# Optimization experiments

Measured on AMD Instinct MI355X. Metric: run time of the kernel, lower is better.

The kernel has to match this reference:

```python
import jax, jax.numpy as jnp
import numpy as np

N, E = 50000, 1000000
IN_DIM, HID, OUT = 2, 32, 16
H1, H2 = 4, 1
NEG_SLOPE = 0.2
LN_EPS = 1e-5


def _glorot(key, shape):
    fan_in, fan_out = shape[0], shape[1]
    lim = (6.0 / (fan_in + fan_out)) ** 0.5
    return jax.random.uniform(key, shape, jnp.float32, -lim, lim)


def layer_norm(x, g, b):
    mu = jnp.mean(x, axis=-1, keepdims=True)
    var = jnp.var(x, axis=-1, keepdims=True)
    return (x - mu) * jax.lax.rsqrt(var + LN_EPS) * g + b


def gatv2_conv(x, src, dst, edge_attr, Wl, bl, Wr, br, We, att, bias, H, C):
    # x: (N, F) -> out: (N, C)  (concat=False: mean over heads)
    n = x.shape[0]
    xl = (x @ Wl + bl).reshape(n, H, C)   # source transform
    xr = (x @ Wr + br).reshape(n, H, C)   # destination transform
    e = (edge_attr @ We).reshape(-1, H, C)  # edge feature transform (no bias)
    # per-edge message, LeakyReLU, attention logit
    m = jax.nn.leaky_relu(xl[src] + xr[dst] + e, NEG_SLOPE)  # (E, H, C)
    logit = jnp.einsum('ehc,hc->eh', m, att)                 # (E, H)
    # scatter softmax grouped by destination node
    amax = jax.ops.segment_max(logit, dst, num_segments=n)    # (N, H)
    ex = jnp.exp(logit - amax[dst])                           # (E, H)
    denom = jax.ops.segment_sum(ex, dst, num_segments=n)      # (N, H)
    alpha = ex / (denom[dst] + 1e-16)                         # (E, H)
    # weighted scatter-aggregate of source features
    out = jax.ops.segment_sum(alpha[:, :, None] * xl[src], dst, num_segments=n)  # (N, H, C)
    return jnp.mean(out, axis=1) + bias


def setup_inputs() -> dict:
    key = jax.random.key(0)
    ks = jax.random.split(key, 16)
    x = jax.random.normal(ks[0], (N, IN_DIM), jnp.float32)
    edge_index = jax.random.randint(ks[1], (2, E), 0, N, jnp.int64)
    edge_attr = jax.random.normal(ks[2], (E, 1), jnp.float32)
    inp = {
        'x': x, 'edge_index': edge_index, 'edge_attr': edge_attr,
        # layer 1 (in=2 -> H1*HID)
        'W1l': _glorot(ks[3], (IN_DIM, H1 * HID)), 'b1l': jnp.zeros((H1 * HID,), jnp.float32),
        'W1r': _glorot(ks[4], (IN_DIM, H1 * HID)), 'b1r': jnp.zeros((H1 * HID,), jnp.float32),
        'We1': _glorot(ks[5], (1, H1 * HID)),
        'att1': _glorot(ks[6], (H1, HID)),
        'bias1': jnp.zeros((HID,), jnp.float32),
        'g1': jnp.ones((HID,), jnp.float32), 'beta1': jnp.zeros((HID,), jnp.float32),
        # layer 2 (HID -> H2*OUT)
        'W2l': _glorot(ks[7], (HID, H2 * OUT)), 'b2l': jnp.zeros((H2 * OUT,), jnp.float32),
        'W2r': _glorot(ks[8], (HID, H2 * OUT)), 'b2r': jnp.zeros((H2 * OUT,), jnp.float32),
        'We2': _glorot(ks[9], (1, H2 * OUT)),
        'att2': _glorot(ks[10], (H2, OUT)),
        'bias2': jnp.zeros((OUT,), jnp.float32),
        'g2': jnp.ones((OUT,), jnp.float32), 'beta2': jnp.zeros((OUT,), jnp.float32),
    }
    return inp


def reference(x, edge_index, edge_attr, W1l, b1l, W1r, b1r, We1, att1, bias1, g1, beta1,
              W2l, b2l, W2r, b2r, We2, att2, bias2, g2, beta2):
    src, dst = edge_index[0], edge_index[1]
    h = gatv2_conv(x, src, dst, edge_attr, W1l, b1l, W1r, b1r, We1, att1, bias1, H1, HID)
    h = jax.nn.elu(layer_norm(h, g1, beta1))  # dropout p=0.0 -> identity
    z = gatv2_conv(h, src, dst, edge_attr, W2l, b2l, W2r, b2r, We2, att2, bias2, H2, OUT)
    return layer_norm(z, g2, beta2)
```

## Files before the change

kernel.cpp:

```cpp
#include <hip/hip_runtime.h>
#include <hip/hip_bf16.h>
#include <math.h>

typedef __hip_bfloat16 bf16;

__device__ __forceinline__ float b2f(bf16 v) { return __bfloat162float(v); }
__device__ __forceinline__ bf16  f2b(float v) { return __float2bfloat16(v); }

template<int F32>
__device__ __forceinline__ float ldf(const void* p, int i) {
    return F32 ? ((const float*)p)[i] : b2f(((const bf16*)p)[i]);
}
template<int F32>
__device__ __forceinline__ void ldx(const void* x, int s, float& x0, float& x1) {
    if (F32) { float2 v = ((const float2*)x)[s]; x0 = v.x; x1 = v.y; }
    else {
        unsigned u = ((const unsigned*)x)[s];
        x0 = __uint_as_float((u & 0xFFFFu) << 16);
        x1 = __uint_as_float(u & 0xFFFF0000u);
    }
}
__device__ __forceinline__ unsigned f2b_hi(float f) {
    unsigned u = __float_as_uint(f);
    u += 0x7FFFu + ((u >> 16) & 1u);
    return u & 0xFFFF0000u;
}
template<int P4>
__device__ __forceinline__ void ldrec(const void* csr, int k, int& s, float& a) {
    if (P4) {
        unsigned u = ((const unsigned*)csr)[k];
        s = (int)(u & 0xFFFFu);
        a = __uint_as_float(u & 0xFFFF0000u);
    } else {
        uint2 r = ((const uint2*)csr)[k];
        s = (int)r.x;
        a = __uint_as_float(r.y);
    }
}
__device__ __forceinline__ float sclamp(float v, float lim) {
    return fminf(fmaxf(v, -lim), lim);
}
template<int CTRL>
__device__ __forceinline__ float dpp_add(float v) {
    int t = __builtin_amdgcn_update_dpp(0, __float_as_int(v), CTRL, 0xF, 0xF, true);
    return v + __int_as_float(t);
}
__device__ __forceinline__ float red16(float v) {
    v = dpp_add<0xB1>(v);
    v = dpp_add<0x4E>(v);
    v = dpp_add<0x124>(v);
    v = dpp_add<0x128>(v);
    return v;
}

#define NEG_SLOPE 0.2f
#define LN_EPS 1e-5f
#define SCAN_TILE 1024
#define ACHUNK 4096

__device__ __forceinline__ int ld_idx(const int* ei, long long pos, int is64, int N) {
    int v = is64 ? ei[2 * pos] : ei[pos];
    return min(max(v, 0), N - 1);
}
__device__ __forceinline__ int calc_is64(const int* ei) {
    int hi = 0, nz = 0;
    #pragma unroll
    for (int i = 0; i < 8; ++i) { hi |= ei[2 * i + 1]; nz |= ei[2 * i]; }
    return (hi == 0 && nz != 0) ? 1 : 0;
}


__global__ __launch_bounds__(256) void histb_kernel(const int* __restrict__ ei,
                                                    const unsigned short* __restrict__ xu,
                                                    int E, int N, int* __restrict__ flags,
                                                    int* __restrict__ bcnt) {
    __shared__ int c[256];
    int tid = threadIdx.x;
    c[tid] = 0;
    int is64 = calc_is64(ei);
    if (blockIdx.x == 0 && tid == 0) {
        flags[0] = is64;
        int pl = 0;
        for (int i = 0; i < 32; ++i) {
            unsigned ex = (xu[2 * i] >> 7) & 0xFF;
            if (ex >= 100 && ex <= 140) pl++;
        }
        flags[1] = (pl >= 24) ? 0 : 1;
    }
    __syncthreads();
    int i0 = blockIdx.x * ACHUNK;
    int iend = min(i0 + ACHUNK, E);
    for (int i = i0 + tid; i < iend; i += 256)
        atomicAdd(&c[ld_idx(ei, (long long)E + i, is64, N) >> 8], 1);
    __syncthreads();
    if (c[tid]) atomicAdd(&bcnt[tid], c[tid]);
}

__global__ void scanb_kernel(const int* __restrict__ bcnt, int* __restrict__ bbase,
                             int* __restrict__ bcursor, int* __restrict__ rowptr,
                             int N, int E) {
    __shared__ int s[256];
    int tid = threadIdx.x;
    int v = bcnt[tid];
    s[tid] = v;
    __syncthreads();
    for (int off = 1; off < 256; off <<= 1) {
        int u = (tid >= off) ? s[tid - off] : 0;
        __syncthreads();
        s[tid] += u;
        __syncthreads();
    }
    int excl = s[tid] - v;
    bbase[tid] = excl;
    bcursor[tid] = excl;
    if (tid == 255) { bbase[256] = s[255]; rowptr[N] = E; }
}

template<int F32>
__device__ void bina_body(const int* __restrict__ ei, const void* __restrict__ attr,
                          int E, int N, int is64, int* __restrict__ bcursor,
                          uint2* __restrict__ binned) {
    __shared__ int cnt[256], incl[256], cur[256];
    __shared__ uint2 stage[ACHUNK];
    int tid = threadIdx.x;
    cnt[tid] = 0;
    __syncthreads();
    int i0 = blockIdx.x * ACHUNK;
    int iend = min(i0 + ACHUNK, E);
    for (int i = i0 + tid; i < iend; i += 256)
        atomicAdd(&cnt[ld_idx(ei, (long long)E + i, is64, N) >> 8], 1);
    __syncthreads();
    incl[tid] = cnt[tid];
    __syncthreads();
    for (int off = 1; off < 256; off <<= 1) {
        int u = (tid >= off) ? incl[tid - off] : 0;
        __syncthreads();
        incl[tid] += u;
        __syncthreads();
    }
    cur[tid] = incl[tid] - cnt[tid];
    __syncthreads();
    for (int i = i0 + tid; i < iend; i += 256) {
        int d = ld_idx(ei, (long long)E + i, is64, N);
        int s = ld_idx(ei, (long long)i, is64, N);
        float a = ldf<F32>(attr, i);
        int p = atomicAdd(&cur[d >> 8], 1);
        stage[p] = make_uint2((unsigned)s | ((unsigned)(d & 255) << 16), f2b_hi(a));
    }
    __syncthreads();
    int c = cnt[tid];
    if (c > 0) {
        int start = incl[tid] - c;
        int g = atomicAdd(&bcursor[tid], c);
        for (int j = 0; j < c; ++j) binned[g + j] = stage[start + j];
    }
}

__global__ __launch_bounds__(256) void bina_kernel(const int* __restrict__ ei,
                                                   const void* __restrict__ attr,
                                                   int E, int N, const int* __restrict__ flags,
                                                   int* __restrict__ bcursor,
                                                   uint2* __restrict__ binned) {
    if (flags[1]) bina_body<1>(ei, attr, E, N, flags[0], bcursor, binned);
    else          bina_body<0>(ei, attr, E, N, flags[0], bcursor, binned);
}

__global__ __launch_bounds__(256) void passb_kernel(const uint2* __restrict__ binned,
                                                    const int* __restrict__ bbase,
                                                    int* __restrict__ rowptr,
                                                    unsigned* __restrict__ csr, int N) {
    __shared__ int nc[256], incl[256], cur[256];
    int b = blockIdx.x, tid = threadIdx.x;
    int base = bbase[b], cntb = bbase[b + 1] - base;
    nc[tid] = 0;
    __syncthreads();
    for (int i = tid; i < cntb; i += 256)
        atomicAdd(&nc[(binned[base + i].x >> 16) & 255], 1);
    __syncthreads();
    incl[tid] = nc[tid];
    __syncthreads();
    for (int off = 1; off < 256; off <<= 1) {
        int u = (tid >= off) ? incl[tid - off] : 0;
        __syncthreads();
        incl[tid] += u;
        __syncthreads();
    }
    int excl = incl[tid] - nc[tid];
    int node = (b << 8) + tid;
    if (node < N) rowptr[node] = base + excl;
    cur[tid] = excl;
    __syncthreads();
    for (int i = tid; i < cntb; i += 256) {
        uint2 r = binned[base + i];
        int p = atomicAdd(&cur[(r.x >> 16) & 255], 1);
        csr[base + p] = r.y | (r.x & 0xFFFFu);
    }
}


__global__ void hist_kernel(const int* __restrict__ ei, const unsigned short* __restrict__ xu,
                            int E, int N, int* __restrict__ flags, int* __restrict__ cnt) {
    int is64 = calc_is64(ei);
    if (blockIdx.x == 0 && threadIdx.x == 0) {
        flags[0] = is64;
        int pl = 0;
        for (int i = 0; i < 32; ++i) {
            unsigned ex = (xu[2 * i] >> 7) & 0xFF;
            if (ex >= 100 && ex <= 140) pl++;
        }
        flags[1] = (pl >= 24) ? 0 : 1;
    }
    int e = blockIdx.x * blockDim.x + threadIdx.x;
    if (e >= E) return;
    atomicAdd(&cnt[ld_idx(ei, (long long)E + e, is64, N)], 1);
}

__global__ __launch_bounds__(256) void scan_partial(const int* __restrict__ cnt,
                                                    int* __restrict__ bsum, int N) {
    __shared__ int wsum[4];
    int b = blockIdx.x, tid = threadIdx.x;
    int base = b * SCAN_TILE + tid * 4;
    int4 v = make_int4(0, 0, 0, 0);
    if (base + 3 < N) v = *(const int4*)(cnt + base);
    else {
        if (base + 0 < N) v.x = cnt[base + 0];
        if (base + 1 < N) v.y = cnt[base + 1];
        if (base + 2 < N) v.z = cnt[base + 2];
    }
    int s = v.x + v.y + v.z + v.w;
    #pragma unroll
    for (int off = 1; off < 64; off <<= 1) s += __shfl_xor(s, off);
    if ((tid & 63) == 0) wsum[tid >> 6] = s;
    __syncthreads();
    if (tid == 0) bsum[b] = wsum[0] + wsum[1] + wsum[2] + wsum[3];
}

__global__ __launch_bounds__(256) void scan_final(int* __restrict__ cnt, int* __restrict__ rowptr,
                                                  const int* __restrict__ bsum, int N, int B) {
    __shared__ int tsum[256];
    __shared__ int bpre[256];
    int b = blockIdx.x, tid = threadIdx.x;
    bpre[tid] = (tid < B) ? bsum[tid] : 0;
    int base = b * SCAN_TILE + tid * 4;
    int4 v = make_int4(0, 0, 0, 0);
    if (base + 3 < N) v = *(const int4*)(cnt + base);
    else {
        if (base + 0 < N) v.x = cnt[base + 0];
        if (base + 1 < N) v.y = cnt[base + 1];
        if (base + 2 < N) v.z = cnt[base + 2];
    }
    tsum[tid] = v.x + v.y + v.z + v.w;
    __syncthreads();
    for (int off = 1; off < 256; off <<= 1) {
        int t = (tid >= off) ? tsum[tid - off] : 0;
        int u = (tid >= off) ? bpre[tid - off] : 0;
        __syncthreads();
        tsum[tid] += t;
        bpre[tid] += u;
        __syncthreads();
    }
    int blockpre = (b == 0) ? 0 : bpre[b - 1];
    int o0 = blockpre + ((tid == 0) ? 0 : tsum[tid - 1]);
    int o1 = o0 + v.x, o2 = o1 + v.y, o3 = o2 + v.z;
    if (base + 3 < N) {
        int4 o = make_int4(o0, o1, o2, o3);
        *(int4*)(rowptr + base) = o;
        *(int4*)(cnt + base) = o;
    } else {
        if (base + 0 < N) { rowptr[base + 0] = o0; cnt[base + 0] = o0; }
        if (base + 1 < N) { rowptr[base + 1] = o1; cnt[base + 1] = o1; }
        if (base + 2 < N) { rowptr[base + 2] = o2; cnt[base + 2] = o2; }
    }
    if (b == 0 && tid == 255) rowptr[N] = bpre[255];
}

template<int F32>
__device__ void scatter_body(const int* __restrict__ ei, const void* __restrict__ attr,
                             int E, int N, int is64, int* __restrict__ cursor,
                             uint2* __restrict__ csr) {
    int e = blockIdx.x * blockDim.x + threadIdx.x;
    if (e >= E) return;
    int d = ld_idx(ei, (long long)E + e, is64, N);
    int s = ld_idx(ei, (long long)e, is64, N);
    float av = ldf<F32>(attr, e);
    int pos = atomicAdd(&cursor[d], 1);
    csr[pos] = make_uint2((unsigned)s, __float_as_uint(av));
}

__global__ void scatter_kernel(const int* __restrict__ ei, const void* __restrict__ attr,
                               int E, int N, const int* __restrict__ flags,
                               int* __restrict__ cursor, uint2* __restrict__ csr) {
    if (flags[1]) scatter_body<1>(ei, attr, E, N, flags[0], cursor, csr);
    else          scatter_body<0>(ei, attr, E, N, flags[0], cursor, csr);
}


template<int F32, int P4>
__device__ void agg1_body(
    const int* __restrict__ rowptr, const void* __restrict__ csr,
    const void* __restrict__ x,
    const void* W1l, const void* b1l, const void* W1r, const void* b1r,
    const void* We1, const void* att1, const void* bias1, const void* g1v, const void* beta1,
    bf16* __restrict__ hout, int N) {
    int w0 = __builtin_amdgcn_readfirstlane((blockIdx.x * blockDim.x + threadIdx.x) >> 6);
    int NW = (gridDim.x * blockDim.x) >> 6;
    int lane = threadIdx.x & 63;
    int h = lane >> 4, q = lane & 15;
    int ja = h * 32 + q, jb = ja + 16;

    float wlaA = ldf<F32>(W1l, ja),      wlaB = ldf<F32>(W1l, jb);
    float wlbA = ldf<F32>(W1l, 128 + ja), wlbB = ldf<F32>(W1l, 128 + jb);
    float wraA = ldf<F32>(W1r, ja),      wraB = ldf<F32>(W1r, jb);
    float wrbA = ldf<F32>(W1r, 128 + ja), wrbB = ldf<F32>(W1r, 128 + jb);
    float blA = ldf<F32>(b1l, ja), blB = ldf<F32>(b1l, jb);
    float brA = ldf<F32>(b1r, ja), brB = ldf<F32>(b1r, jb);
    float weA = ldf<F32>(We1, ja), weB = ldf<F32>(We1, jb);
    float atA = ldf<F32>(att1, ja), atB = ldf<F32>(att1, jb);
    float aa4A = 0.4f * atA, aa4B = 0.4f * atB;
    float blbrA = blA + brA, blbrB = blB + brB;
    float P0 = 0.6f * red16(atA * wlaA + atB * wlaB);
    float P1 = 0.6f * red16(atA * wlbA + atB * wlbB);
    float Pw = 0.6f * red16(atA * weA + atB * weB);
    float Q0 = 0.6f * red16(atA * wraA + atB * wraB);
    float Q1 = 0.6f * red16(atA * wrbA + atB * wrbB);
    float Qc = 0.6f * red16(atA * blbrA + atB * blbrB);
    float biasA = ldf<F32>(bias1, q), biasB = ldf<F32>(bias1, q + 16);
    float gA = ldf<F32>(g1v, q), gB = ldf<F32>(g1v, q + 16);
    float beA = ldf<F32>(beta1, q), beB = ldf<F32>(beta1, q + 16);

    for (int n = w0; n < N; n += NW) {
        int beg = rowptr[n], end = rowptr[n + 1];
        float xd0, xd1;
        ldx<F32>(x, n, xd0, xd1);
        float cA = fmaf(xd0, wraA, fmaf(xd1, wrbA, blbrA));
        float cB = fmaf(xd0, wraB, fmaf(xd1, wrbB, blbrB));
        float Kn = fmaf(xd0, Q0, fmaf(xd1, Q1, Qc));
        float S = 0.f, Sx0 = 0.f, Sx1 = 0.f;

        auto edge = [&](float xs0, float xs1, float a) {
            float zA = fmaf(xs0, wlaA, fmaf(xs1, wlbA, fmaf(a, weA, cA)));
            float zB = fmaf(xs0, wlaB, fmaf(xs1, wlbB, fmaf(a, weB, cB)));
            float pabs = red16(fmaf(fabsf(zA), aa4A, fabsf(zB) * aa4B));
            float p = sclamp(fmaf(xs0, P0, fmaf(xs1, P1, fmaf(a, Pw, Kn))) + pabs, 60.f);
            float e = __expf(p);
            S += e;
            Sx0 = fmaf(e, xs0, Sx0);
            Sx1 = fmaf(e, xs1, Sx1);
        };

        int k = beg;
        for (; k + 4 <= end; k += 4) {
            int s0, s1, s2, s3;
            float a0, a1, a2, a3;
            ldrec<P4>(csr, k, s0, a0);
            ldrec<P4>(csr, k + 1, s1, a1);
            ldrec<P4>(csr, k + 2, s2, a2);
            ldrec<P4>(csr, k + 3, s3, a3);
            float p0, p1, q0, q1, r0, r1, t0, t1;
            ldx<F32>(x, s0, p0, p1);
            ldx<F32>(x, s1, q0, q1);
            ldx<F32>(x, s2, r0, r1);
            ldx<F32>(x, s3, t0, t1);
            edge(p0, p1, a0);
            edge(q0, q1, a1);
            edge(r0, r1, a2);
            edge(t0, t1, a3);
        }
        for (; k < end; ++k) {
            int s0; float a0;
            ldrec<P4>(csr, k, s0, a0);
            float p0, p1;
            ldx<F32>(x, s0, p0, p1);
            edge(p0, p1, a0);
        }

        float inv = 1.0f / (S + 1e-16f);
        float R = S * inv, U0 = Sx0 * inv, U1 = Sx1 * inv;
        float outA = fmaf(U0, wlaA, fmaf(U1, wlbA, R * blA));
        float outB = fmaf(U0, wlaB, fmaf(U1, wlbB, R * blB));
        outA += __shfl_xor(outA, 16); outA += __shfl_xor(outA, 32);
        outB += __shfl_xor(outB, 16); outB += __shfl_xor(outB, 32);
        float valA = fmaf(0.25f, outA, biasA);
        float valB = fmaf(0.25f, outB, biasB);
        float mu = red16(valA + valB) * (1.f / 32.f);
        float dA = valA - mu, dB = valB - mu;
        float var = red16(dA * dA + dB * dB) * (1.f / 32.f);
        float rs = rsqrtf(var + LN_EPS);
        float yA = fmaf(dA * rs, gA, beA);
        float yB = fmaf(dB * rs, gB, beB);
        float hA = yA > 0.f ? yA : expm1f(yA);
        float hB = yB > 0.f ? yB : expm1f(yB);
        if (lane < 16) {
            hout[n * 32 + q]      = f2b(hA);
            hout[n * 32 + 16 + q] = f2b(hB);
        }
    }
}

template<int P4>
__global__ __launch_bounds__(256) void agg1_kernel(
    const int* __restrict__ flags,
    const int* __restrict__ rowptr, const void* __restrict__ csr,
    const void* __restrict__ x,
    const void* W1l, const void* b1l, const void* W1r, const void* b1r,
    const void* We1, const void* att1, const void* bias1, const void* g1v, const void* beta1,
    bf16* __restrict__ hout, int N) {
    if (flags[1]) agg1_body<1, P4>(rowptr, csr, x, W1l, b1l, W1r, b1r,
                                   We1, att1, bias1, g1v, beta1, hout, N);
    else          agg1_body<0, P4>(rowptr, csr, x, W1l, b1l, W1r, b1r,
                                   We1, att1, bias1, g1v, beta1, hout, N);
}


template<int F32>
__device__ void node2_body(bf16* __restrict__ hbuf, float* wl, float* wr,
                           const void* W2l, const void* b2l, const void* W2r, const void* b2r,
                           int N) {
    __shared__ float bl[16], br[16];
    int tid = threadIdx.x;
    for (int i = tid; i < 512; i += 256) { wl[i] = ldf<F32>(W2l, i); wr[i] = ldf<F32>(W2r, i); }
    if (tid < 16) { bl[tid] = ldf<F32>(b2l, tid); br[tid] = ldf<F32>(b2r, tid); }
    __syncthreads();
    int n = blockIdx.x * blockDim.x + tid;
    if (n >= N) return;
    float hv[32];
    #pragma unroll
    for (int c = 0; c < 32; ++c) hv[c] = b2f(hbuf[n * 32 + c]);
    float accl[16], accr[16];
    #pragma unroll
    for (int o = 0; o < 16; ++o) { accl[o] = bl[o]; accr[o] = br[o]; }
    #pragma unroll
    for (int c = 0; c < 32; ++c) {
        #pragma unroll
        for (int o = 0; o < 16; ++o) {
            accl[o] = fmaf(hv[c], wl[c * 16 + o], accl[o]);
            accr[o] = fmaf(hv[c], wr[c * 16 + o], accr[o]);
        }
    }
    #pragma unroll
    for (int o = 0; o < 16; ++o) {
        hbuf[n * 32 + o]      = f2b(accl[o]);
        hbuf[n * 32 + 16 + o] = f2b(accr[o]);
    }
}

__global__ __launch_bounds__(256) void node2_kernel(
    const int* __restrict__ flags, bf16* __restrict__ hbuf,
    const void* W2l, const void* b2l, const void* W2r, const void* b2r, int N) {
    __shared__ float wl[512], wr[512];
    if (flags[1]) node2_body<1>(hbuf, wl, wr, W2l, b2l, W2r, b2r, N);
    else          node2_body<0>(hbuf, wl, wr, W2l, b2l, W2r, b2r, N);
}


template<int F32, int P4>
__device__ void agg2_body(
    const int* __restrict__ rowptr, const void* __restrict__ csr,
    const bf16* __restrict__ h2,
    const void* We2, const void* att2, const void* bias2, const void* g2v, const void* beta2,
    void* __restrict__ out, int N) {
    int w0 = __builtin_amdgcn_readfirstlane((blockIdx.x * blockDim.x + threadIdx.x) >> 6);
    int NW = (gridDim.x * blockDim.x) >> 6;
    int lane = threadIdx.x & 63;
    int g = lane >> 4, t = lane & 15;

    float we = ldf<F32>(We2, t), at = ldf<F32>(att2, t);
    float bia = ldf<F32>(bias2, t), gg = ldf<F32>(g2v, t), bb = ldf<F32>(beta2, t);

    for (int n = w0; n < N; n += NW) {
        int beg = rowptr[n], end = rowptr[n + 1];
        float xr = b2f(h2[n * 32 + 16 + t]);

        float S = 0.f, A = 0.f;
        auto edge = [&](float v, float a) {
            float m = fmaf(a, we, v + xr);
            m = fmaxf(m, NEG_SLOPE * m);
            float p = sclamp(red16(m * at), 60.f);
            float e = __expf(p);
            S += e;
            A = fmaf(e, v, A);
        };
        int k = beg + g;
        for (; k + 4 < end; k += 8) {
            int s0, s1; float a0, a1;
            ldrec<P4>(csr, k, s0, a0);
            ldrec<P4>(csr, k + 4, s1, a1);
            float v0 = b2f(h2[s0 * 32 + t]);
            float v1 = b2f(h2[s1 * 32 + t]);
            edge(v0, a0);
            edge(v1, a1);
        }
        if (k < end) {
            int s0; float a0;
            ldrec<P4>(csr, k, s0, a0);
            edge(b2f(h2[s0 * 32 + t]), a0);
        }
        S += __shfl_xor(S, 16); S += __shfl_xor(S, 32);
        A += __shfl_xor(A, 16); A += __shfl_xor(A, 32);
        float val = A / (S + 1e-16f) + bia;

        float mu = red16(val) * (1.f / 16.f);
        float d = val - mu;
        float var = red16(d * d) * (1.f / 16.f);
        float y = fmaf(d * rsqrtf(var + LN_EPS), gg, bb);
        if (lane < 16) {
            if (F32) ((float*)out)[n * 16 + t] = y;
            else     ((bf16*)out)[n * 16 + t] = f2b(y);
        }
    }
}

template<int P4>
__global__ __launch_bounds__(256) void agg2_kernel(
    const int* __restrict__ flags,
    const int* __restrict__ rowptr, const void* __restrict__ csr,
    const bf16* __restrict__ h2,
    const void* We2, const void* att2, const void* bias2, const void* g2v, const void* beta2,
    void* __restrict__ out, int N) {
    if (flags[1]) agg2_body<1, P4>(rowptr, csr, h2, We2, att2, bias2, g2v, beta2, out, N);
    else          agg2_body<0, P4>(rowptr, csr, h2, We2, att2, bias2, g2v, beta2, out, N);
}


static inline size_t align256(size_t x) { return (x + 255) & ~size_t(255); }

extern "C" void kernel_launch(void* const* d_in, const int* in_sizes, int n_in,
                              void* d_out, int out_size, void* d_ws, size_t ws_size,
                              hipStream_t stream) {
    const void* x     = d_in[0];
    const int*  ei    = (const int*)d_in[1];
    const void* eattr = d_in[2];
    const void* W1l   = d_in[3];
    const void* b1l   = d_in[4];
    const void* W1r   = d_in[5];
    const void* b1r   = d_in[6];
    const void* We1   = d_in[7];
    const void* att1  = d_in[8];
    const void* bias1 = d_in[9];
    const void* g1    = d_in[10];
    const void* beta1 = d_in[11];
    const void* W2l   = d_in[12];
    const void* b2l   = d_in[13];
    const void* W2r   = d_in[14];
    const void* b2r   = d_in[15];
    const void* We2   = d_in[16];
    const void* att2  = d_in[17];
    const void* bias2 = d_in[18];
    const void* g2    = d_in[19];
    const void* beta2 = d_in[20];

    const int N = in_sizes[0] / 2;
    const int E = in_sizes[2];
    const bool p4 = (N <= 65536);
    const int EB = (E + ACHUNK - 1) / ACHUNK;

    char* ws = (char*)d_ws;
    size_t off = 0;
    int* flags   = (int*)(ws + off); off += align256(sizeof(int) * 2);
    int* bcnt    = (int*)(ws + off); off += align256(sizeof(int) * 1024);
    int* bbase   = (int*)(ws + off); off += align256(sizeof(int) * 257);
    int* bcursor = (int*)(ws + off); off += align256(sizeof(int) * 256);
    int* rowptr  = (int*)(ws + off); off += align256(sizeof(int) * (size_t)(N + 1));
    void* csr    = (void*)(ws + off); off += align256((p4 ? 4u : 8u) * (size_t)E);
    char* big    = (ws + off);
    uint2* binned = (uint2*)big;
    int*   cnt    = (int*)big;
    bf16*  hbuf   = (bf16*)big;

    if (p4) {
        hipMemsetAsync(bcnt, 0, sizeof(int) * 256, stream);
        histb_kernel<<<EB, 256, 0, stream>>>(ei, (const unsigned short*)x, E, N, flags, bcnt);
        scanb_kernel<<<1, 256, 0, stream>>>(bcnt, bbase, bcursor, rowptr, N, E);
        bina_kernel<<<EB, 256, 0, stream>>>(ei, eattr, E, N, flags, bcursor, binned);
        passb_kernel<<<(N + 255) >> 8, 256, 0, stream>>>(binned, bbase, rowptr, (unsigned*)csr, N);
    } else {
        cnt = (int*)big;
        hbuf = (bf16*)(big + align256(sizeof(int) * (size_t)N));
        const int B = (N + SCAN_TILE - 1) / SCAN_TILE;
        hipMemsetAsync(cnt, 0, sizeof(int) * (size_t)N, stream);
        hist_kernel<<<(E + 255) / 256, 256, 0, stream>>>(ei, (const unsigned short*)x, E, N, flags, cnt);
        scan_partial<<<B, 256, 0, stream>>>(cnt, bcnt, N);
        scan_final<<<B, 256, 0, stream>>>(cnt, rowptr, bcnt, N, B);
        scatter_kernel<<<(E + 255) / 256, 256, 0, stream>>>(ei, eattr, E, N, flags, cnt, (uint2*)csr);
    }

    if (p4) agg1_kernel<1><<<2048, 256, 0, stream>>>(flags, rowptr, csr, x,
                                                     W1l, b1l, W1r, b1r, We1, att1,
                                                     bias1, g1, beta1, hbuf, N);
    else    agg1_kernel<0><<<2048, 256, 0, stream>>>(flags, rowptr, csr, x,
                                                     W1l, b1l, W1r, b1r, We1, att1,
                                                     bias1, g1, beta1, hbuf, N);

    node2_kernel<<<(N + 255) / 256, 256, 0, stream>>>(flags, hbuf, W2l, b2l, W2r, b2r, N);

    if (p4) agg2_kernel<1><<<2048, 256, 0, stream>>>(flags, rowptr, csr, hbuf,
                                                     We2, att2, bias2, g2, beta2, d_out, N);
    else    agg2_kernel<0><<<2048, 256, 0, stream>>>(flags, rowptr, csr, hbuf,
                                                     We2, att2, bias2, g2, beta2, d_out, N);
}
```

Baseline: 225.0 us.

## Use exp2 with log2e-folded weights, unroll edge loop by 8, enlarge grids

Folds log2(e) into the precomputed attention coefficients so the per-edge exponential becomes a native exp2 call, which removes a multiply per edge. The clamp bound is scaled to match. The layer-1 edge loop now handles 8 edges per iteration instead of 4, putting more gathers in flight. Both aggregation kernels launch 3072 blocks instead of 2048. These are several small independent tweaks, and the wider unroll adds register pressure.

Result: slower. 234.9 us (+4.4%).

```diff
diff --git a/kernel.cpp b/kernel.cpp
--- a/kernel.cpp
+++ b/kernel.cpp
@@ -6,6 +6,8 @@
 
 __device__ __forceinline__ float b2f(bf16 v) { return __bfloat162float(v); }
 __device__ __forceinline__ bf16  f2b(float v) { return __float2bfloat16(v); }
+
+#define LOG2E 1.44269504088896340736f
 
 template<int F32>
 __device__ __forceinline__ float ldf(const void* p, int i) {
@@ -316,14 +318,15 @@
     float brA = ldf<F32>(b1r, ja), brB = ldf<F32>(b1r, jb);
     float weA = ldf<F32>(We1, ja), weB = ldf<F32>(We1, jb);
     float atA = ldf<F32>(att1, ja), atB = ldf<F32>(att1, jb);
-    float aa4A = 0.4f * atA, aa4B = 0.4f * atB;
+    float aa4A = (0.4f * LOG2E) * atA, aa4B = (0.4f * LOG2E) * atB;
     float blbrA = blA + brA, blbrB = blB + brB;
-    float P0 = 0.6f * red16(atA * wlaA + atB * wlaB);
-    float P1 = 0.6f * red16(atA * wlbA + atB * wlbB);
-    float Pw = 0.6f * red16(atA * weA + atB * weB);
-    float Q0 = 0.6f * red16(atA * wraA + atB * wraB);
-    float Q1 = 0.6f * red16(atA * wrbA + atB * wrbB);
-    float Qc = 0.6f * red16(atA * blbrA + atB * blbrB);
+    const float c6 = 0.6f * LOG2E;
+    float P0 = c6 * red16(atA * wlaA + atB * wlaB);
+    float P1 = c6 * red16(atA * wlbA + atB * wlbB);
+    float Pw = c6 * red16(atA * weA + atB * weB);
+    float Q0 = c6 * red16(atA * wraA + atB * wraB);
+    float Q1 = c6 * red16(atA * wrbA + atB * wrbB);
+    float Qc = c6 * red16(atA * blbrA + atB * blbrB);
     float biasA = ldf<F32>(bias1, q), biasB = ldf<F32>(bias1, q + 16);
     float gA = ldf<F32>(g1v, q), gB = ldf<F32>(g1v, q + 16);
     float beA = ldf<F32>(beta1, q), beB = ldf<F32>(beta1, q + 16);
@@ -341,30 +344,22 @@
             float zA = fmaf(xs0, wlaA, fmaf(xs1, wlbA, fmaf(a, weA, cA)));
             float zB = fmaf(xs0, wlaB, fmaf(xs1, wlbB, fmaf(a, weB, cB)));
             float pabs = red16(fmaf(fabsf(zA), aa4A, fabsf(zB) * aa4B));
-            float p = sclamp(fmaf(xs0, P0, fmaf(xs1, P1, fmaf(a, Pw, Kn))) + pabs, 60.f);
-            float e = __expf(p);
+            float p = sclamp(fmaf(xs0, P0, fmaf(xs1, P1, fmaf(a, Pw, Kn))) + pabs, 86.f);
+            float e = __builtin_exp2f(p);
             S += e;
             Sx0 = fmaf(e, xs0, Sx0);
             Sx1 = fmaf(e, xs1, Sx1);
         };
 
         int k = beg;
-        for (; k + 4 <= end; k += 4) {
-            int s0, s1, s2, s3;
-            float a0, a1, a2, a3;
-            ldrec<P4>(csr, k, s0, a0);
-            ldrec<P4>(csr, k + 1, s1, a1);
-            ldrec<P4>(csr, k + 2, s2, a2);
-            ldrec<P4>(csr, k + 3, s3, a3);
-            float p0, p1, q0, q1, r0, r1, t0, t1;
-            ldx<F32>(x, s0, p0, p1);
-            ldx<F32>(x, s1, q0, q1);
-            ldx<F32>(x, s2, r0, r1);
-            ldx<F32>(x, s3, t0, t1);
-            edge(p0, p1, a0);
-            edge(q0, q1, a1);
-            edge(r0, r1, a2);
-            edge(t0, t1, a3);
+        for (; k + 8 <= end; k += 8) {
+            int ss[8]; float aa[8], xx0[8], xx1[8];
+            #pragma unroll
+            for (int j = 0; j < 8; ++j) ldrec<P4>(csr, k + j, ss[j], aa[j]);
+            #pragma unroll
+            for (int j = 0; j < 8; ++j) ldx<F32>(x, ss[j], xx0[j], xx1[j]);
+            #pragma unroll
+            for (int j = 0; j < 8; ++j) edge(xx0[j], xx1[j], aa[j]);
         }
         for (; k < end; ++k) {
             int s0; float a0;
@@ -464,7 +459,7 @@
     int lane = threadIdx.x & 63;
     int g = lane >> 4, t = lane & 15;
 
-    float we = ldf<F32>(We2, t), at = ldf<F32>(att2, t);
+    float we = ldf<F32>(We2, t), at = LOG2E * ldf<F32>(att2, t);
     float bia = ldf<F32>(bias2, t), gg = ldf<F32>(g2v, t), bb = ldf<F32>(beta2, t);
 
     for (int n = w0; n < N; n += NW) {
@@ -475,8 +470,8 @@
         auto edge = [&](float v, float a) {
             float m = fmaf(a, we, v + xr);
             m = fmaxf(m, NEG_SLOPE * m);
-            float p = sclamp(red16(m * at), 60.f);
-            float e = __expf(p);
+            float p = sclamp(red16(m * at), 86.f);
+            float e = __builtin_exp2f(p);
             S += e;
             A = fmaf(e, v, A);
         };
@@ -584,17 +579,17 @@
         scatter_kernel<<<(E + 255) / 256, 256, 0, stream>>>(ei, eattr, E, N, flags, cnt, (uint2*)csr);
     }
 
-    if (p4) agg1_kernel<1><<<2048, 256, 0, stream>>>(flags, rowptr, csr, x,
+    if (p4) agg1_kernel<1><<<3072, 256, 0, stream>>>(flags, rowptr, csr, x,
                                                      W1l, b1l, W1r, b1r, We1, att1,
                                                      bias1, g1, beta1, hbuf, N);
-    else    agg1_kernel<0><<<2048, 256, 0, stream>>>(flags, rowptr, csr, x,
+    else    agg1_kernel<0><<<3072, 256, 0, stream>>>(flags, rowptr, csr, x,
                                                      W1l, b1l, W1r, b1r, We1, att1,
                                                      bias1, g1, beta1, hbuf, N);
 
     node2_kernel<<<(N + 255) / 256, 256, 0, stream>>>(flags, hbuf, W2l, b2l, W2r, b2r, N);
 
-    if (p4) agg2_kernel<1><<<2048, 256, 0, stream>>>(flags, rowptr, csr, hbuf,
+    if (p4) agg2_kernel<1><<<3072, 256, 0, stream>>>(flags, rowptr, csr, hbuf,
                                                      We2, att2, bias2, g2, beta2, d_out, N);
-    else    agg2_kernel<0><<<2048, 256, 0, stream>>>(flags, rowptr, csr, hbuf,
+    else    agg2_kernel<0><<<3072, 256, 0, stream>>>(flags, rowptr, csr, hbuf,
                                                      We2, att2, bias2, g2, beta2, d_out, N);
 }
```
